# Kernel tuning notes

Measured on AMD Instinct MI355X. Metric: run time of the kernel, lower is better.

The kernel has to match this reference:

```python
import jax, jax.numpy as jnp
import numpy as np

R_MAX = 5.0
NUM_BESSEL = 8
P_CUT = 5
AVG_NEIGH = 10.0
N_NODES, N_EDGES, N_GRAPHS, N_ELEM, CH = 16384, 65536, 64, 10, 128
L_OF_M = np.array([0,1,1,1,2,2,2,2,2,3,3,3,3,3,3,3])  # l index of each of the 16 sh components
L_POOL = jnp.asarray((np.arange(4)[:, None] == L_OF_M[None, :]).astype(np.float32))  # [4,16]


def spherical_harmonics(u):
    # real spherical harmonics, component normalization (||Y_l|| = sqrt(2l+1)), l=0..3; u: [E,3] unit
    x, y, z = u[..., 0], u[..., 1], u[..., 2]
    s3, s15, s5 = 3.0**0.5, 15.0**0.5, 5.0**0.5
    s35_8, s105, s21_8, s7 = (35.0/8.0)**0.5, 105.0**0.5, (21.0/8.0)**0.5, 7.0**0.5
    x2, y2, z2 = x*x, y*y, z*z
    Y = [jnp.ones_like(x),
         s3*x, s3*y, s3*z,
         s15*x*y, s15*y*z, 0.5*s5*(3.0*z2 - 1.0), s15*x*z, 0.5*s15*(x2 - y2),
         s35_8*y*(3.0*x2 - y2), s105*x*y*z, s21_8*y*(5.0*z2 - 1.0), 0.5*s7*z*(5.0*z2 - 3.0),
         s21_8*x*(5.0*z2 - 1.0), 0.5*s105*z*(x2 - y2), s35_8*x*(x2 - 3.0*y2)]
    return jnp.stack(Y, axis=-1)  # [E,16]


def radial_embedding(r):
    # Bessel basis * polynomial envelope cutoff (p=5); r: [E,1]
    n = jnp.arange(1, NUM_BESSEL + 1, dtype=r.dtype)
    bessel = (2.0 / R_MAX)**0.5 * jnp.sin(n * jnp.pi * r / R_MAX) / r  # [E,8]
    u = r / R_MAX
    p = float(P_CUT)
    f = 1.0 - 0.5*(p+1.0)*(p+2.0)*u**p + p*(p+2.0)*u**(p+1.0) - 0.5*p*(p+1.0)*u**(p+2.0)
    f = f * (u < 1.0).astype(r.dtype)
    return bessel * f


def setup_inputs() -> dict:
    key = jax.random.key(0)
    ks = iter(jax.random.split(key, 32))
    species = jax.random.randint(next(ks), (N_NODES,), 0, N_ELEM)
    x = jax.nn.one_hot(species, N_ELEM, dtype=jnp.float32)
    pos = jax.random.uniform(next(ks), (N_NODES, 3), dtype=jnp.float32) * 4.0
    edge_index = jax.random.randint(next(ks), (2, N_EDGES), 0, N_NODES)
    batch_idx = jnp.sort(jax.random.randint(next(ks), (N_NODES,), 0, N_GRAPHS))
    def rn(shape):
        return jax.random.normal(next(ks), shape, jnp.float32)
    return dict(x=x, pos=pos,
                W_embed=rn((N_ELEM, CH)), W_up=rn((2, CH, CH)),
                Wr0=rn((2, NUM_BESSEL, 64)), Wr1=rn((2, 64, 64)), Wr2=rn((2, 64, 64)), Wr3=rn((2, 64, 4*CH)),
                W_lin=rn((2, 4, CH, CH)), W_skip=rn((2, N_ELEM, CH, CH)),
                Wp1=rn((2, N_ELEM, CH)), Wp2=rn((2, N_ELEM, 4, CH)), Wp3=rn((2, N_ELEM, 4, CH)),
                W_prodlin=rn((2, CH, CH)),
                edge_index=edge_index, batch_idx=batch_idx)


def reference(x, pos, W_embed, W_up, Wr0, Wr1, Wr2, Wr3, W_lin, W_skip, Wp1, Wp2, Wp3, W_prodlin, edge_index, batch_idx):
    j, i = edge_index[0], edge_index[1]
    vec = pos[j] - pos[i]                                        # [E,3]
    length = jnp.sqrt(jnp.sum(vec * vec, axis=-1, keepdims=True) + 1e-12)
    edge_sh = spherical_harmonics(vec / length)                  # [E,16]
    edge_feats = radial_embedding(length)                        # [E,8]
    node_feats = (x @ W_embed) / (N_ELEM**0.5)                   # [N,128] (0e)
    for t in range(2):
        # residual skip: FullyConnectedTensorProduct(node_feats 0e x node_attrs 0e -> 0e)
        sc = jnp.einsum('nz,nk,zkl->nl', x, node_feats, W_skip[t]) / ((CH * N_ELEM)**0.5)
        up = (node_feats @ W_up[t]) / (CH**0.5)                  # linear_up
        # radial MLP -> per-edge tensor-product path weights [E,4,128] (one path per l)
        h = jax.nn.silu((edge_feats @ Wr0[t]) / (NUM_BESSEL**0.5))
        h = jax.nn.silu((h @ Wr1[t]) / 8.0)
        h = jax.nn.silu((h @ Wr2[t]) / 8.0)
        tpw = ((h @ Wr3[t]) / 8.0).reshape(-1, 4, CH)
        # CG tensor product 0e x (0e+1o+2e+3o) -> per-edge message, scatter to receivers
        msg_e = edge_sh[:, :, None] * up[j][:, None, :] * tpw[:, L_OF_M, :]   # [E,16,128]
        msg = jax.ops.segment_sum(msg_e, i, num_segments=N_NODES) / AVG_NEIGH  # [N,16,128]
        # equivariant linear (weights shared within each l)
        A = jnp.einsum('nmk,mkl->nml', msg, W_lin[t][L_OF_M]) / (CH**0.5)     # [N,16,128]
        # product basis: symmetric contraction to 0e (correlations 1..3), element-dependent weights
        A0 = A[:, 0, :]                                                        # [N,128]
        inv2 = jnp.einsum('nmk,lm->nlk', A * A, L_POOL)                        # [N,4,128]  A_l . A_l
        w1 = x @ Wp1[t]
        w2 = jnp.einsum('nz,zlk->nlk', x, Wp2[t])
        w3 = jnp.einsum('nz,zlk->nlk', x, Wp3[t])
        b = w1 * A0 + jnp.sum(w2 * inv2, axis=1) + jnp.sum(w3 * inv2, axis=1) * A0
        node_feats = (b @ W_prodlin[t]) / (CH**0.5) + sc
    # scatter_mean over graphs
    ones = jnp.ones((node_feats.shape[0],), node_feats.dtype)
    cnt = jax.ops.segment_sum(ones, batch_idx, num_segments=N_GRAPHS)
    env = jax.ops.segment_sum(node_feats, batch_idx, num_segments=N_GRAPHS)
    return env / jnp.maximum(cnt, 1.0)[:, None]
```

## Files before the change

kernel.cpp:

```cpp
#include <hip/hip_runtime.h>

typedef unsigned short u16;
typedef unsigned int   u32;
typedef __attribute__((ext_vector_type(8))) short short8;
typedef __attribute__((ext_vector_type(4))) float float4v;

#define N_NODES  16384
#define N_EDGES  65536
#define N_GRAPHS 64

__device__ __forceinline__ float bf(u16 u) { return __uint_as_float(((u32)u) << 16); }
__device__ __forceinline__ u16 fb(float f) {
    u32 b = __float_as_uint(f);
    b += 0x7FFFu + ((b >> 16) & 1u);
    return (u16)(b >> 16);
}
__device__ __forceinline__ float silu_f(float x) { return x / (1.f + __expf(-x)); }

__device__ __constant__ int RBc[16] = {0, 16384,16385,16386, 65536,65537,65538,65539,65540,
                                       147456,147457,147458,147459,147460,147461,147462};
__device__ __constant__ int RSc[16] = {1,3,3,3,5,5,5,5,5,7,7,7,7,7,7,7};

__global__ void k_zero(float* p, int n) {
    int i = blockIdx.x * 256 + threadIdx.x;
    if (i < n) p[i] = 0.f;
}

__global__ void k_detect(const void* x, int* flag) {
    __shared__ int f;
    if (threadIdx.x == 0) f = 0;
    __syncthreads();
    const u16* p = (const u16*)x;
    for (int i = threadIdx.x; i < 4096; i += 256)
        if (p[i] == 0x3F80u && (i & 1) == 0) f = 1;
    __syncthreads();
    if (threadIdx.x == 0) *flag = f;
}

struct CvtArgs { const void* src[12]; int n[12]; };
__global__ void k_convert(CvtArgs a, u16* dst, const int* flag) {
    int fl = *flag;
    size_t base = 0;
    int stride = gridDim.x * 256;
    for (int q = 0; q < 12; q++) {
        int n = a.n[q];
        for (int i = blockIdx.x * 256 + threadIdx.x; i < n; i += stride) {
            u16 v;
            if (fl) v = ((const u16*)a.src[q])[i];
            else    v = fb(((const float*)a.src[q])[i]);
            if (q == 6) {
                int slab = i >> 14, rem = i & 16383, kk = rem >> 7, nn = rem & 127;
                dst[base + slab * 16384 + nn * 128 + kk] = v;
            } else if (q == 3 || q == 4) {
                int tq = i >> 12, rem = i & 4095, kk = rem >> 6, nn = rem & 63;
                dst[base + tq * 4096 + nn * 64 + kk] = v;
            } else if (q == 5) {
                int tq = i >> 15, rem = i & 32767, kk = rem >> 9, nn = rem & 511;
                dst[base + tq * 32768 + nn * 64 + kk] = v;
            } else if (q == 1 || q == 11) {
                int tq = i >> 14, rem = i & 16383, kk = rem >> 7, k = rem & 127;
                dst[base + tq * 16384 + k * 128 + kk] = v;
            } else if (q == 7) {
                int tq = i >= 163840 ? 1 : 0, rem = i - tq * 163840;
                int sp = rem >> 14, r2 = rem & 16383, kk = r2 >> 7, k = r2 & 127;
                dst[base + ((size_t)tq * 10 + sp) * 16384 + k * 128 + kk] = v;
            } else {
                dst[base + i] = v;
            }
        }
        base += n;
    }
}

__global__ __launch_bounds__(256) void k_species(const void* x, int* species, int* shist,
                                                 const int* flag) {
    __shared__ int lh[10];
    int tid = threadIdx.x;
    if (tid < 10) lh[tid] = 0;
    __syncthreads();
    int n = blockIdx.x * 256 + tid;
    int sp = 0;
    if (*flag) {
        const u16* xp = (const u16*)x + (size_t)n * 10;
        for (int z = 0; z < 10; z++)
            if (bf(xp[z]) > 0.5f) { sp = z; break; }
    } else {
        const float* xp = (const float*)x + (size_t)n * 10;
        for (int z = 0; z < 10; z++)
            if (xp[z] > 0.5f) { sp = z; break; }
    }
    species[n] = sp;
    atomicAdd(&lh[sp], 1);
    __syncthreads();
    if (tid < 10) atomicAdd(&shist[tid], lh[tid]);
}

__global__ __launch_bounds__(256) void k_embed(const int* species, const u16* Wemb, float* nf) {
    int i = blockIdx.x * 256 + threadIdx.x;
    int n = i >> 7, k = i & 127;
    nf[i] = bf(Wemb[species[n] * 128 + k]) * 0.31622776601683794f;
}

__global__ void k_spscan(const int* shist, int* spoffs, int* spcursor) {
    if (threadIdx.x == 0) {
        int run = 0;
        for (int s = 0; s < 10; s++) { spoffs[s] = run; spcursor[s] = run; run += shist[s]; }
        spoffs[10] = run;
    }
}

__global__ __launch_bounds__(256) void k_spsort(const int* species, int* spcursor, int* perm) {
    __shared__ int lcnt[10], lbase[10], lrank[10];
    int tid = threadIdx.x;
    if (tid < 10) { lcnt[tid] = 0; lrank[tid] = 0; }
    __syncthreads();
    int n = blockIdx.x * 256 + tid;
    int sp = species[n];
    atomicAdd(&lcnt[sp], 1);
    __syncthreads();
    if (tid < 10) lbase[tid] = atomicAdd(&spcursor[tid], lcnt[tid]);
    __syncthreads();
    int r = atomicAdd(&lrank[sp], 1);
    perm[lbase[sp] + r] = n;
}

__global__ __launch_bounds__(256) void k_prep_edges(const int* eidx, const void* pos,
                                                    float* esh, float* ef, int* hist,
                                                    const int* flag) {
    int e = blockIdx.x * 256 + threadIdx.x;
    int j = eidx[e], i = eidx[N_EDGES + e];
    float vx, vy, vz;
    if (*flag) {
        const u16* p = (const u16*)pos;
        vx = bf(p[j * 3 + 0]) - bf(p[i * 3 + 0]);
        vy = bf(p[j * 3 + 1]) - bf(p[i * 3 + 1]);
        vz = bf(p[j * 3 + 2]) - bf(p[i * 3 + 2]);
    } else {
        const float* p = (const float*)pos;
        vx = p[j * 3 + 0] - p[i * 3 + 0];
        vy = p[j * 3 + 1] - p[i * 3 + 1];
        vz = p[j * 3 + 2] - p[i * 3 + 2];
    }
    float r = sqrtf(vx * vx + vy * vy + vz * vz + 1e-12f);
    float rinv = 1.f / r;
    float X = vx * rinv, Y = vy * rinv, Z = vz * rinv;
    float x2 = X * X, y2 = Y * Y, z2 = Z * Z;
    const float s3 = 1.7320508075688772f, s15 = 3.872983346207417f, s5 = 2.23606797749979f;
    const float s35_8 = 2.091650066335189f, s105 = 10.246950765959598f;
    const float s21_8 = 1.6201851746019651f, s7 = 2.6457513110645907f;
    float Yh[16];
    Yh[0] = 1.f; Yh[1] = s3 * X; Yh[2] = s3 * Y; Yh[3] = s3 * Z;
    Yh[4] = s15 * X * Y; Yh[5] = s15 * Y * Z; Yh[6] = 0.5f * s5 * (3.f * z2 - 1.f);
    Yh[7] = s15 * X * Z; Yh[8] = 0.5f * s15 * (x2 - y2);
    Yh[9] = s35_8 * Y * (3.f * x2 - y2); Yh[10] = s105 * X * Y * Z;
    Yh[11] = s21_8 * Y * (5.f * z2 - 1.f); Yh[12] = 0.5f * s7 * Z * (5.f * z2 - 3.f);
    Yh[13] = s21_8 * X * (5.f * z2 - 1.f); Yh[14] = 0.5f * s105 * Z * (x2 - y2);
    Yh[15] = s35_8 * X * (x2 - 3.f * y2);
#pragma unroll
    for (int m = 0; m < 16; m++) esh[e * 16 + m] = Yh[m];

    float u = r * 0.2f;
    float fc = 0.f;
    if (u < 1.f) {
        float u2 = u * u, u4 = u2 * u2, u5 = u4 * u, u6 = u5 * u, u7 = u6 * u;
        fc = 1.f - 21.f * u5 + 35.f * u6 - 15.f * u7;
    }
    const float pref = 0.6324555320336759f;
#pragma unroll
    for (int nn = 1; nn <= 8; nn++)
        ef[e * 8 + nn - 1] = pref * sinf((float)nn * 3.14159265358979323846f * u) * rinv * fc;

    atomicAdd(&hist[i], 1);
}

__global__ __launch_bounds__(1024) void k_scan(const int* hist, int* offs, int* cursor) {
    __shared__ int part[1024];
    int t = threadIdx.x;
    int base = t * 16;
    int v[16]; int s = 0;
#pragma unroll
    for (int q = 0; q < 16; q++) { v[q] = hist[base + q]; s += v[q]; }
    part[t] = s;
    __syncthreads();
    for (int d = 1; d < 1024; d <<= 1) {
        int add = (t >= d) ? part[t - d] : 0;
        __syncthreads();
        part[t] += add;
        __syncthreads();
    }
    int run = part[t] - s;
#pragma unroll
    for (int q = 0; q < 16; q++) { offs[base + q] = run; cursor[base + q] = run; run += v[q]; }
    if (t == 1023) offs[16384] = run;
}

__global__ __launch_bounds__(256) void k_sort(const int* eidx, int* cursor, int* sorted) {
    int e = blockIdx.x * 256 + threadIdx.x;
    int i = eidx[N_EDGES + e];
    int p = atomicAdd(&cursor[i], 1);
    sorted[p] = e;
}

__global__ __launch_bounds__(256) void k_upsc(int t, const float* nf, const int* perm,
                                              const int* spoffs, const u16* WupT,
                                              const u16* WskipT, u16* up, float* sc) {
    __shared__ u16 wu[16384];
    __shared__ u16 wsk[16384];
    int s = blockIdx.y;
    int rstart = spoffs[s] + blockIdx.x * 64;
    int rend = spoffs[s + 1];
    if (rstart >= rend) return;
    int tid = threadIdx.x;
    const u16* wg1 = WupT + (size_t)t * 16384;
    const u16* wg2 = WskipT + ((size_t)t * 10 + s) * 16384;
#pragma unroll
    for (int p = 0; p < 8; p++) {
        int slot = p * 256 + tid;
        int nt = slot >> 8, ks = (slot >> 6) & 3, ln = slot & 63;
        int nn = nt * 16 + (ln & 15), k0 = ks * 32 + (ln >> 4) * 8;
        *(uint4*)&wu[slot * 8]  = *(const uint4*)&wg1[nn * 128 + k0];
        *(uint4*)&wsk[slot * 8] = *(const uint4*)&wg2[nn * 128 + k0];
    }
    __syncthreads();

    int wave = tid >> 6, lane = tid & 63;
    int m16 = lane & 15, quad = lane >> 4;
    int arow = rstart + wave * 16 + m16;
    int anode = perm[arow < rend ? arow : rstart];
    short8 afr[4];
#pragma unroll
    for (int ks = 0; ks < 4; ks++) {
        const float* ap = nf + (size_t)anode * 128 + ks * 32 + quad * 8;
        short8 v;
#pragma unroll
        for (int q = 0; q < 8; q++) v[q] = (short)fb(ap[q]);
        afr[ks] = v;
    }

    float4v accU[8], accS[8];
#pragma unroll
    for (int nt = 0; nt < 8; nt++) {
        accU[nt] = (float4v){0.f, 0.f, 0.f, 0.f};
        accS[nt] = (float4v){0.f, 0.f, 0.f, 0.f};
#pragma unroll
        for (int ks = 0; ks < 4; ks++) {
            short8 b1 = *(const short8*)&wu[((nt * 4 + ks) * 64 + lane) * 8];
            short8 b2 = *(const short8*)&wsk[((nt * 4 + ks) * 64 + lane) * 8];
            accU[nt] = __builtin_amdgcn_mfma_f32_16x16x32_bf16(afr[ks], b1, accU[nt], 0, 0, 0);
            accS[nt] = __builtin_amdgcn_mfma_f32_16x16x32_bf16(afr[ks], b2, accS[nt], 0, 0, 0);
        }
    }

    int crow0 = rstart + wave * 16 + quad * 4;
    int cnode[4]; int cvalid[4];
#pragma unroll
    for (int r = 0; r < 4; r++) {
        int rr = crow0 + r;
        cvalid[r] = rr < rend;
        cnode[r] = perm[cvalid[r] ? rr : rstart];
    }
#pragma unroll
    for (int nt = 0; nt < 8; nt++) {
        int col = nt * 16 + m16;
#pragma unroll
        for (int r = 0; r < 4; r++) {
            if (cvalid[r]) {
                up[(size_t)cnode[r] * 128 + col] = fb(accU[nt][r] * 0.08838834764831845f);
                sc[(size_t)cnode[r] * 128 + col] = accS[nt][r] * 0.027950849718747373f;
            }
        }
    }
}

#define HS 68
__global__ __launch_bounds__(64) void k_radial(int t, const float* ef, const u16* Wr0,
                                               const u16* Wr1T, const u16* Wr2T,
                                               const u16* Wr3T, u16* tpw) {
    __shared__ u16 w0s[512];
    __shared__ u16 hbuf[2176];
    int tid = threadIdx.x;
    const u16* w0p = Wr0 + t * 512;
    *(uint4*)&w0s[tid * 8] = *(const uint4*)&w0p[tid * 8];
    __syncthreads();

    int lane = tid;
    int m16 = lane & 15, quad = lane >> 4;
    int E0 = blockIdx.x * 16;
    u16* h0 = &hbuf[0];
    u16* h1 = &hbuf[1088];

    float efv[8];
    {
        const float* ep = ef + (size_t)(E0 + m16) * 8;
        float4 e0 = *(const float4*)ep, e1 = *(const float4*)(ep + 4);
        efv[0] = e0.x; efv[1] = e0.y; efv[2] = e0.z; efv[3] = e0.w;
        efv[4] = e1.x; efv[5] = e1.y; efv[6] = e1.z; efv[7] = e1.w;
    }
#pragma unroll
    for (int o = 0; o < 16; o++) {
        int oc = quad * 16 + o;
        float a = 0.f;
#pragma unroll
        for (int b = 0; b < 8; b++) a += efv[b] * bf(w0s[b * 64 + oc]);
        h0[m16 * HS + oc] = fb(silu_f(a * 0.35355339059327373f));
    }
    __syncthreads();

    const u16* w1p = Wr1T + t * 4096;
    short8 afr[2];
    afr[0] = *(const short8*)&h0[m16 * HS + quad * 8];
    afr[1] = *(const short8*)&h0[m16 * HS + 32 + quad * 8];
    {
        float4v acc[4];
#pragma unroll
        for (int nt = 0; nt < 4; nt++) {
            acc[nt] = (float4v){0.f, 0.f, 0.f, 0.f};
#pragma unroll
            for (int ks = 0; ks < 2; ks++) {
                short8 bfr = *(const short8*)&w1p[(nt * 16 + m16) * 64 + ks * 32 + quad * 8];
                acc[nt] = __builtin_amdgcn_mfma_f32_16x16x32_bf16(afr[ks], bfr, acc[nt], 0, 0, 0);
            }
        }
#pragma unroll
        for (int nt = 0; nt < 4; nt++)
#pragma unroll
            for (int r = 0; r < 4; r++)
                h1[(quad * 4 + r) * HS + nt * 16 + m16] = fb(silu_f(acc[nt][r] * 0.125f));
    }
    __syncthreads();

    const u16* w2p = Wr2T + t * 4096;
    afr[0] = *(const short8*)&h1[m16 * HS + quad * 8];
    afr[1] = *(const short8*)&h1[m16 * HS + 32 + quad * 8];
    {
        float4v acc[4];
#pragma unroll
        for (int nt = 0; nt < 4; nt++) {
            acc[nt] = (float4v){0.f, 0.f, 0.f, 0.f};
#pragma unroll
            for (int ks = 0; ks < 2; ks++) {
                short8 bfr = *(const short8*)&w2p[(nt * 16 + m16) * 64 + ks * 32 + quad * 8];
                acc[nt] = __builtin_amdgcn_mfma_f32_16x16x32_bf16(afr[ks], bfr, acc[nt], 0, 0, 0);
            }
        }
#pragma unroll
        for (int nt = 0; nt < 4; nt++)
#pragma unroll
            for (int r = 0; r < 4; r++)
                h0[(quad * 4 + r) * HS + nt * 16 + m16] = fb(silu_f(acc[nt][r] * 0.125f));
    }
    __syncthreads();

    const u16* w3p = Wr3T + t * 32768;
    afr[0] = *(const short8*)&h0[m16 * HS + quad * 8];
    afr[1] = *(const short8*)&h0[m16 * HS + 32 + quad * 8];
    u16* stw = &hbuf[0];
    for (int cc = 0; cc < 4; cc++) {
#pragma unroll
        for (int nt8 = 0; nt8 < 8; nt8++) {
            int nt = cc * 8 + nt8;
            float4v a3 = (float4v){0.f, 0.f, 0.f, 0.f};
#pragma unroll
            for (int ks = 0; ks < 2; ks++) {
                short8 bfr = *(const short8*)&w3p[(nt * 16 + m16) * 64 + ks * 32 + quad * 8];
                a3 = __builtin_amdgcn_mfma_f32_16x16x32_bf16(afr[ks], bfr, a3, 0, 0, 0);
            }
#pragma unroll
            for (int r = 0; r < 4; r++)
                stw[(quad * 4 + r) * 136 + nt8 * 16 + m16] = fb(a3[r] * 0.125f);
        }
        __syncthreads();
#pragma unroll
        for (int st = 0; st < 4; st++) {
            int edge = st * 4 + quad;
            uint4 v = *(const uint4*)&stw[edge * 136 + m16 * 8];
            *(uint4*)&tpw[(size_t)(E0 + edge) * 512 + cc * 128 + m16 * 8] = v;
        }
        __syncthreads();
    }
}

__global__ __launch_bounds__(256) void k_msg(const int* offs, const int* sorted,
                                             const int* eidx, const float* esh,
                                             const u16* up, const u16* tpw, u16* msgA) {
    const int LM[16] = {0,1,1,1,2,2,2,2,2,3,3,3,3,3,3,3};
    int tid = threadIdx.x;
    int nsub = tid >> 5;
    int kq = tid & 31;
    int k4 = kq * 4;
    int n = blockIdx.x * 8 + nsub;

    float acc[16][4];
#pragma unroll
    for (int m = 0; m < 16; m++)
#pragma unroll
        for (int q = 0; q < 4; q++) acc[m][q] = 0.f;
    int s = offs[n], e1 = offs[n + 1];
    for (int idx = s; idx < e1; idx++) {
        int e = sorted[idx];
        int j = eidx[e];
        ushort4 uu = *(const ushort4*)(up + (size_t)j * 128 + k4);
        float u0 = bf(uu.x), u1 = bf(uu.y), u2 = bf(uu.z), u3 = bf(uu.w);
        float4 sA = *(const float4*)(esh + (size_t)e * 16);
        float4 sB = *(const float4*)(esh + (size_t)e * 16 + 4);
        float4 sC = *(const float4*)(esh + (size_t)e * 16 + 8);
        float4 sD = *(const float4*)(esh + (size_t)e * 16 + 12);
        float sh[16] = {sA.x, sA.y, sA.z, sA.w, sB.x, sB.y, sB.z, sB.w,
                        sC.x, sC.y, sC.z, sC.w, sD.x, sD.y, sD.z, sD.w};
        float p[4][4];
#pragma unroll
        for (int l = 0; l < 4; l++) {
            ushort4 tp = *(const ushort4*)(tpw + (size_t)e * 512 + l * 128 + k4);
            p[l][0] = u0 * bf(tp.x); p[l][1] = u1 * bf(tp.y);
            p[l][2] = u2 * bf(tp.z); p[l][3] = u3 * bf(tp.w);
        }
#pragma unroll
        for (int m = 0; m < 16; m++) {
            int l = LM[m];
            acc[m][0] += sh[m] * p[l][0]; acc[m][1] += sh[m] * p[l][1];
            acc[m][2] += sh[m] * p[l][2]; acc[m][3] += sh[m] * p[l][3];
        }
    }
#pragma unroll
    for (int m = 0; m < 16; m++) {
        int row = RBc[m] + n * RSc[m];
        ushort4 o;
        o.x = fb(acc[m][0] * 0.1f); o.y = fb(acc[m][1] * 0.1f);
        o.z = fb(acc[m][2] * 0.1f); o.w = fb(acc[m][3] * 0.1f);
        *(ushort4*)(msgA + (size_t)row * 128 + k4) = o;
    }
}

__global__ __launch_bounds__(256) void k_gemmA(int t, u16* msgA, const u16* WlinT) {
    __shared__ u16 wfr[16384];
    int b = blockIdx.x;
    int l, rb0;
    if (b < 256)       { l = 0; rb0 = b * 64; }
    else if (b < 1024) { l = 1; rb0 = 16384  + (b - 256)  * 64; }
    else if (b < 2304) { l = 2; rb0 = 65536  + (b - 1024) * 64; }
    else               { l = 3; rb0 = 147456 + (b - 2304) * 64; }
    int tid = threadIdx.x;
    const u16* wg = WlinT + ((size_t)t * 4 + l) * 16384;
#pragma unroll
    for (int p = 0; p < 8; p++) {
        int slot = p * 256 + tid;
        int nt = slot >> 8, ks = (slot >> 6) & 3, ln = slot & 63;
        int nn = nt * 16 + (ln & 15), k0 = ks * 32 + (ln >> 4) * 8;
        *(uint4*)&wfr[slot * 8] = *(const uint4*)&wg[nn * 128 + k0];
    }
    __syncthreads();

    int wave = tid >> 6, lane = tid & 63;
    int m16 = lane & 15, quad = lane >> 4;
    int rowa = rb0 + wave * 16 + m16;
    const u16* ap = msgA + (size_t)rowa * 128 + quad * 8;
    short8 afr[4];
#pragma unroll
    for (int ks = 0; ks < 4; ks++) afr[ks] = *(const short8*)(ap + ks * 32);

    float4v acc[8];
#pragma unroll
    for (int nt = 0; nt < 8; nt++) acc[nt] = (float4v){0.f, 0.f, 0.f, 0.f};
#pragma unroll
    for (int nt = 0; nt < 8; nt++)
#pragma unroll
        for (int ks = 0; ks < 4; ks++) {
            short8 bfr = *(const short8*)&wfr[((nt * 4 + ks) * 64 + lane) * 8];
            acc[nt] = __builtin_amdgcn_mfma_f32_16x16x32_bf16(afr[ks], bfr, acc[nt], 0, 0, 0);
        }

    const float sAc = 0.08838834764831845f;
    int rowc = rb0 + wave * 16 + quad * 4;
#pragma unroll
    for (int nt = 0; nt < 8; nt++)
#pragma unroll
        for (int r = 0; r < 4; r++)
            msgA[(size_t)(rowc + r) * 128 + nt * 16 + m16] = fb(acc[nt][r] * sAc);
}

__global__ __launch_bounds__(128) void k_bprod_b(int t, const u16* Ag, const int* species,
                                                 const u16* Wp1, const u16* Wp2, const u16* Wp3,
                                                 u16* bvec) {
    const int LM[16] = {0,1,1,1,2,2,2,2,2,3,3,3,3,3,3,3};
    int n = blockIdx.x, k = threadIdx.x;
    int sp = species[n];
    float Am[16];
#pragma unroll
    for (int m = 0; m < 16; m++)
        Am[m] = bf(Ag[(size_t)(RBc[m] + n * RSc[m]) * 128 + k]);
    float A0 = Am[0];
    float inv2[4] = {0.f, 0.f, 0.f, 0.f};
#pragma unroll
    for (int m = 0; m < 16; m++) inv2[LM[m]] += Am[m] * Am[m];
    float w1 = bf(Wp1[((size_t)t * 10 + sp) * 128 + k]);
    float s2 = 0.f, s3v = 0.f;
#pragma unroll
    for (int l = 0; l < 4; l++) {
        float w2 = bf(Wp2[(((size_t)t * 10 + sp) * 4 + l) * 128 + k]);
        float w3 = bf(Wp3[(((size_t)t * 10 + sp) * 4 + l) * 128 + k]);
        s2 += w2 * inv2[l];
        s3v += w3 * inv2[l];
    }
    bvec[(size_t)n * 128 + k] = fb(w1 * A0 + s2 + s3v * A0);
}

__global__ __launch_bounds__(256) void k_gemm_nf(int t, const u16* bvec, const u16* WplT,
                                                 const float* sc, float* nf) {
    __shared__ u16 wfr[16384];
    int rb0 = blockIdx.x * 64;
    int tid = threadIdx.x;
    const u16* wg = WplT + (size_t)t * 16384;
#pragma unroll
    for (int p = 0; p < 8; p++) {
        int slot = p * 256 + tid;
        int nt = slot >> 8, ks = (slot >> 6) & 3, ln = slot & 63;
        int nn = nt * 16 + (ln & 15), k0 = ks * 32 + (ln >> 4) * 8;
        *(uint4*)&wfr[slot * 8] = *(const uint4*)&wg[nn * 128 + k0];
    }
    __syncthreads();

    int wave = tid >> 6, lane = tid & 63;
    int m16 = lane & 15, quad = lane >> 4;
    int rowa = rb0 + wave * 16 + m16;
    const u16* ap = bvec + (size_t)rowa * 128 + quad * 8;
    short8 afr[4];
#pragma unroll
    for (int ks = 0; ks < 4; ks++) afr[ks] = *(const short8*)(ap + ks * 32);

    float4v acc[8];
#pragma unroll
    for (int nt = 0; nt < 8; nt++) acc[nt] = (float4v){0.f, 0.f, 0.f, 0.f};
#pragma unroll
    for (int nt = 0; nt < 8; nt++)
#pragma unroll
        for (int ks = 0; ks < 4; ks++) {
            short8 bfr = *(const short8*)&wfr[((nt * 4 + ks) * 64 + lane) * 8];
            acc[nt] = __builtin_amdgcn_mfma_f32_16x16x32_bf16(afr[ks], bfr, acc[nt], 0, 0, 0);
        }

    const float sAc = 0.08838834764831845f;
    int rowc = rb0 + wave * 16 + quad * 4;
#pragma unroll
    for (int nt = 0; nt < 8; nt++) {
        int col = nt * 16 + m16;
#pragma unroll
        for (int r = 0; r < 4; r++) {
            size_t idx = (size_t)(rowc + r) * 128 + col;
            nf[idx] = acc[nt][r] * sAc + sc[idx];
        }
    }
}

__global__ __launch_bounds__(128) void k_reduce(const float* nf, const int* batch,
                                                float* env, float* cnt) {
    int k = threadIdx.x;
    int n0 = blockIdx.x * 8;
    float run = 0.f;
    int c = 0;
    int gp = batch[n0];
    for (int nn = 0; nn < 8; nn++) {
        int n = n0 + nn;
        int g = batch[n];
        if (g != gp) {
            atomicAdd(&env[gp * 128 + k], run);
            if (k == 0) atomicAdd(&cnt[gp], (float)c);
            run = 0.f; c = 0; gp = g;
        }
        run += nf[(size_t)n * 128 + k];
        c++;
    }
    atomicAdd(&env[gp * 128 + k], run);
    if (k == 0) atomicAdd(&cnt[gp], (float)c);
}

__global__ void k_final(const float* env, const float* cnt, float* out) {
    int i = blockIdx.x * 256 + threadIdx.x;
    if (i < N_GRAPHS * 128) out[i] = env[i] / fmaxf(cnt[i >> 7], 1.f);
}

extern "C" void kernel_launch(void* const* d_in, const int* in_sizes, int n_in,
                              void* d_out, int out_size, void* d_ws, size_t ws_size,
                              hipStream_t stream) {
    (void)in_sizes; (void)n_in; (void)out_size; (void)ws_size;
    const void* x    = d_in[0];
    const void* pos  = d_in[1];
    const int* eidx  = (const int*)d_in[14];
    const int* batch = (const int*)d_in[15];

    char* base = (char*)d_ws;
    size_t cur = 0;
    auto alloc = [&](size_t bytes) -> void* {
        void* p = base + cur;
        cur = (cur + bytes + 255) & ~(size_t)255;
        return p;
    };
    int*   flag    = (int*)alloc(4);
    u16*   cvt     = (u16*)alloc((size_t)631552 * 2);
    int*   species = (int*)alloc((size_t)N_NODES * 4);
    int*   shist   = (int*)alloc(64);
    int*   spoffs  = (int*)alloc(64);
    int*   spcursor= (int*)alloc(64);
    int*   perm    = (int*)alloc((size_t)N_NODES * 4);
    int*   hist    = (int*)alloc((size_t)N_NODES * 4);
    int*   offs    = (int*)alloc((size_t)(N_NODES + 1) * 4);
    int*   cursor  = (int*)alloc((size_t)N_NODES * 4);
    int*   sorted  = (int*)alloc((size_t)N_EDGES * 4);
    float* env     = (float*)alloc((size_t)N_GRAPHS * 128 * 4);
    float* cnt     = (float*)alloc((size_t)N_GRAPHS * 4);
    float* nf      = (float*)alloc((size_t)N_NODES * 128 * 4);
    u16*   up      = (u16*)alloc((size_t)N_NODES * 128 * 2);
    u16*   bvec    = (u16*)alloc((size_t)N_NODES * 128 * 2);
    float* sc      = (float*)alloc((size_t)N_NODES * 128 * 4);
    float* ef      = (float*)alloc((size_t)N_EDGES * 8 * 4);
    float* esh     = (float*)alloc((size_t)N_EDGES * 16 * 4);
    u16*   tpw     = (u16*)alloc((size_t)N_EDGES * 512 * 2);
    u16*   msgA    = (u16*)alloc((size_t)262144 * 128 * 2);

    static const int cn[12] = {1280, 32768, 1024, 8192, 8192, 65536,
                               131072, 327680, 2560, 10240, 10240, 32768};
    CvtArgs ca;
    size_t off[13]; off[0] = 0;
    for (int q = 0; q < 12; q++) { ca.src[q] = d_in[2 + q]; ca.n[q] = cn[q]; off[q + 1] = off[q] + cn[q]; }
    u16* cWemb  = cvt + off[0];
    u16* cWupT  = cvt + off[1];
    u16* cWr0   = cvt + off[2];
    u16* cWr1T  = cvt + off[3];
    u16* cWr2T  = cvt + off[4];
    u16* cWr3T  = cvt + off[5];
    u16* cWlinT = cvt + off[6];
    u16* cWskipT= cvt + off[7];
    u16* cWp1   = cvt + off[8];
    u16* cWp2   = cvt + off[9];
    u16* cWp3   = cvt + off[10];
    u16* cWplT  = cvt + off[11];

    k_detect<<<1, 256, 0, stream>>>(x, flag);
    k_convert<<<256, 256, 0, stream>>>(ca, cvt, flag);
    k_zero<<<64, 256, 0, stream>>>((float*)hist, N_NODES);
    k_zero<<<1, 64, 0, stream>>>((float*)shist, 16);
    k_zero<<<32, 256, 0, stream>>>(env, N_GRAPHS * 128);
    k_zero<<<1, 256, 0, stream>>>(cnt, N_GRAPHS);
    k_species<<<N_NODES / 256, 256, 0, stream>>>(x, species, shist, flag);
    k_embed<<<N_NODES * 128 / 256, 256, 0, stream>>>(species, cWemb, nf);
    k_spscan<<<1, 64, 0, stream>>>(shist, spoffs, spcursor);
    k_spsort<<<N_NODES / 256, 256, 0, stream>>>(species, spcursor, perm);
    k_prep_edges<<<N_EDGES / 256, 256, 0, stream>>>(eidx, pos, esh, ef, hist, flag);
    k_scan<<<1, 1024, 0, stream>>>(hist, offs, cursor);
    k_sort<<<N_EDGES / 256, 256, 0, stream>>>(eidx, cursor, sorted);

    for (int t = 0; t < 2; t++) {
        k_upsc<<<dim3(256, 10), 256, 0, stream>>>(t, nf, perm, spoffs, cWupT, cWskipT, up, sc);
        k_radial<<<N_EDGES / 16, 64, 0, stream>>>(t, ef, cWr0, cWr1T, cWr2T, cWr3T, tpw);
        k_msg<<<N_NODES / 8, 256, 0, stream>>>(offs, sorted, eidx, esh, up, tpw, msgA);
        k_gemmA<<<4096, 256, 0, stream>>>(t, msgA, cWlinT);
        k_bprod_b<<<N_NODES, 128, 0, stream>>>(t, msgA, species, cWp1, cWp2, cWp3, bvec);
        k_gemm_nf<<<N_NODES / 64, 256, 0, stream>>>(t, bvec, cWplT, sc, nf);
    }
    k_reduce<<<N_NODES / 8, 128, 0, stream>>>(nf, batch, env, cnt);
    k_final<<<32, 256, 0, stream>>>(env, cnt, (float*)d_out);
}
```

Measured before the change: 451.6 us.

## Fuse equivariant linear GEMM with product-basis contraction per node tile

```diff
diff --git a/kernel.cpp b/kernel.cpp
--- a/kernel.cpp
+++ b/kernel.cpp
@@ -379,6 +379,7 @@
         __syncthreads();
     }
 }
+#undef HS
 
 __global__ __launch_bounds__(256) void k_msg(const int* offs, const int* sorted,
                                              const int* eidx, const float* esh,
@@ -431,77 +432,84 @@
     }
 }
 
-__global__ __launch_bounds__(256) void k_gemmA(int t, u16* msgA, const u16* WlinT) {
+__global__ __launch_bounds__(256) void k_gemmAb(int t, const u16* msgA, const u16* WlinT,
+                                                const int* species,
+                                                const u16* Wp1, const u16* Wp2, const u16* Wp3,
+                                                u16* bvec) {
     __shared__ u16 wfr[16384];
-    int b = blockIdx.x;
-    int l, rb0;
-    if (b < 256)       { l = 0; rb0 = b * 64; }
-    else if (b < 1024) { l = 1; rb0 = 16384  + (b - 256)  * 64; }
-    else if (b < 2304) { l = 2; rb0 = 65536  + (b - 1024) * 64; }
-    else               { l = 3; rb0 = 147456 + (b - 2304) * 64; }
     int tid = threadIdx.x;
-    const u16* wg = WlinT + ((size_t)t * 4 + l) * 16384;
-#pragma unroll
-    for (int p = 0; p < 8; p++) {
-        int slot = p * 256 + tid;
-        int nt = slot >> 8, ks = (slot >> 6) & 3, ln = slot & 63;
-        int nn = nt * 16 + (ln & 15), k0 = ks * 32 + (ln >> 4) * 8;
-        *(uint4*)&wfr[slot * 8] = *(const uint4*)&wg[nn * 128 + k0];
-    }
-    __syncthreads();
-
     int wave = tid >> 6, lane = tid & 63;
     int m16 = lane & 15, quad = lane >> 4;
-    int rowa = rb0 + wave * 16 + m16;
-    const u16* ap = msgA + (size_t)rowa * 128 + quad * 8;
-    short8 afr[4];
-#pragma unroll
-    for (int ks = 0; ks < 4; ks++) afr[ks] = *(const short8*)(ap + ks * 32);
-
-    float4v acc[8];
-#pragma unroll
-    for (int nt = 0; nt < 8; nt++) acc[nt] = (float4v){0.f, 0.f, 0.f, 0.f};
-#pragma unroll
-    for (int nt = 0; nt < 8; nt++)
-#pragma unroll
-        for (int ks = 0; ks < 4; ks++) {
-            short8 bfr = *(const short8*)&wfr[((nt * 4 + ks) * 64 + lane) * 8];
-            acc[nt] = __builtin_amdgcn_mfma_f32_16x16x32_bf16(afr[ks], bfr, acc[nt], 0, 0, 0);
-        }
-
+    int n0w = blockIdx.x * 64 + wave * 16;
     const float sAc = 0.08838834764831845f;
-    int rowc = rb0 + wave * 16 + quad * 4;
-#pragma unroll
-    for (int nt = 0; nt < 8; nt++)
-#pragma unroll
-        for (int r = 0; r < 4; r++)
-            msgA[(size_t)(rowc + r) * 128 + nt * 16 + m16] = fb(acc[nt][r] * sAc);
-}
-
-__global__ __launch_bounds__(128) void k_bprod_b(int t, const u16* Ag, const int* species,
-                                                 const u16* Wp1, const u16* Wp2, const u16* Wp3,
-                                                 u16* bvec) {
-    const int LM[16] = {0,1,1,1,2,2,2,2,2,3,3,3,3,3,3,3};
-    int n = blockIdx.x, k = threadIdx.x;
-    int sp = species[n];
-    float Am[16];
-#pragma unroll
-    for (int m = 0; m < 16; m++)
-        Am[m] = bf(Ag[(size_t)(RBc[m] + n * RSc[m]) * 128 + k]);
-    float A0 = Am[0];
-    float inv2[4] = {0.f, 0.f, 0.f, 0.f};
-#pragma unroll
-    for (int m = 0; m < 16; m++) inv2[LM[m]] += Am[m] * Am[m];
-    float w1 = bf(Wp1[((size_t)t * 10 + sp) * 128 + k]);
-    float s2 = 0.f, s3v = 0.f;
+
+    float A0[8][4];
+    float inv2[4][8][4];
+#pragma unroll
+    for (int l = 0; l < 4; l++)
+#pragma unroll
+        for (int nt = 0; nt < 8; nt++)
+#pragma unroll
+            for (int r = 0; r < 4; r++) inv2[l][nt][r] = 0.f;
+
+    const int ms_[4] = {0, 1, 4, 9}, me_[4] = {1, 4, 9, 16};
 #pragma unroll
     for (int l = 0; l < 4; l++) {
-        float w2 = bf(Wp2[(((size_t)t * 10 + sp) * 4 + l) * 128 + k]);
-        float w3 = bf(Wp3[(((size_t)t * 10 + sp) * 4 + l) * 128 + k]);
-        s2 += w2 * inv2[l];
-        s3v += w3 * inv2[l];
-    }
-    bvec[(size_t)n * 128 + k] = fb(w1 * A0 + s2 + s3v * A0);
+        __syncthreads();
+        const u16* wg = WlinT + ((size_t)t * 4 + l) * 16384;
+#pragma unroll
+        for (int p = 0; p < 8; p++) {
+            int slot = p * 256 + tid;
+            int nt = slot >> 8, ks = (slot >> 6) & 3, ln = slot & 63;
+            int nn = nt * 16 + (ln & 15), k0 = ks * 32 + (ln >> 4) * 8;
+            *(uint4*)&wfr[slot * 8] = *(const uint4*)&wg[nn * 128 + k0];
+        }
+        __syncthreads();
+#pragma unroll
+        for (int m = ms_[l]; m < me_[l]; m++) {
+            int rowa = RBc[m] + (n0w + m16) * RSc[m];
+            const u16* ap = msgA + (size_t)rowa * 128 + quad * 8;
+            short8 afr[4];
+#pragma unroll
+            for (int ks = 0; ks < 4; ks++) afr[ks] = *(const short8*)(ap + ks * 32);
+#pragma unroll
+            for (int nt = 0; nt < 8; nt++) {
+                float4v acc = (float4v){0.f, 0.f, 0.f, 0.f};
+#pragma unroll
+                for (int ks = 0; ks < 4; ks++) {
+                    short8 bfr = *(const short8*)&wfr[((nt * 4 + ks) * 64 + lane) * 8];
+                    acc = __builtin_amdgcn_mfma_f32_16x16x32_bf16(afr[ks], bfr, acc, 0, 0, 0);
+                }
+#pragma unroll
+                for (int r = 0; r < 4; r++) {
+                    float a = acc[r] * sAc;
+                    if (m == 0) A0[nt][r] = a;
+                    inv2[l][nt][r] += a * a;
+                }
+            }
+        }
+    }
+
+#pragma unroll
+    for (int r = 0; r < 4; r++) {
+        int n = n0w + quad * 4 + r;
+        int sp = species[n];
+        const u16* p1 = Wp1 + ((size_t)t * 10 + sp) * 128;
+        const u16* p2 = Wp2 + ((size_t)t * 10 + sp) * 4 * 128;
+        const u16* p3 = Wp3 + ((size_t)t * 10 + sp) * 4 * 128;
+#pragma unroll
+        for (int nt = 0; nt < 8; nt++) {
+            int ch = nt * 16 + m16;
+            float w1 = bf(p1[ch]);
+            float s2 = 0.f, s3 = 0.f;
+#pragma unroll
+            for (int l = 0; l < 4; l++) {
+                s2 += bf(p2[l * 128 + ch]) * inv2[l][nt][r];
+                s3 += bf(p3[l * 128 + ch]) * inv2[l][nt][r];
+            }
+            bvec[(size_t)n * 128 + ch] = fb(w1 * A0[nt][r] + s2 + s3 * A0[nt][r]);
+        }
+    }
 }
 
 __global__ __launch_bounds__(256) void k_gemm_nf(int t, const u16* bvec, const u16* WplT,
@@ -652,8 +660,8 @@
         k_upsc<<<dim3(256, 10), 256, 0, stream>>>(t, nf, perm, spoffs, cWupT, cWskipT, up, sc);
         k_radial<<<N_EDGES / 16, 64, 0, stream>>>(t, ef, cWr0, cWr1T, cWr2T, cWr3T, tpw);
         k_msg<<<N_NODES / 8, 256, 0, stream>>>(offs, sorted, eidx, esh, up, tpw, msgA);
-        k_gemmA<<<4096, 256, 0, stream>>>(t, msgA, cWlinT);
-        k_bprod_b<<<N_NODES, 128, 0, stream>>>(t, msgA, species, cWp1, cWp2, cWp3, bvec);
+        k_gemmAb<<<N_NODES / 64, 256, 0, stream>>>(t, msgA, cWlinT, species,
+                                                   cWp1, cWp2, cWp3, bvec);
         k_gemm_nf<<<N_NODES / 64, 256, 0, stream>>>(t, bvec, cWplT, sc, nf);
     }
     k_reduce<<<N_NODES / 8, 128, 0, stream>>>(nf, batch, env, cnt);
```

New measurement: 475.4 us. +5.3%, slower.
